# Kernel optimization log

Hardware: AMD Instinct MI355X
Metric: run time of the kernel (lower is better)

## Reference

```python
import jax, jax.numpy as jnp
import numpy as np

B, L, D = 4, 2048, 512
DK = D // 2
DH = 256.0  # scaling denominator


def _skew(QE):
    # QE: [B, L, M] with M == L (relative position logits via skewing trick)
    b, l, m = QE.shape
    pad = jnp.zeros((b, l, 1), QE.dtype)
    cat = jnp.concatenate([pad, QE], axis=2)      # [B, L, M+1]
    reshaped = cat.reshape(b, m + 1, l)           # [B, M+1, L]
    return reshaped[:, 1:, :]                     # [B, M, L]


def setup_inputs() -> dict:
    key = jax.random.key(0)
    ks = jax.random.split(key, 7)
    return {
        "inputQ": jax.random.normal(ks[0], (B, L, D), jnp.float32),
        "inputK": jax.random.normal(ks[1], (B, L, D), jnp.float32),
        "inputV": jax.random.normal(ks[2], (B, L, D), jnp.float32),
        "Wq": jax.random.normal(ks[3], (D, DK), jnp.float32) * 0.02,
        "Wk": jax.random.normal(ks[4], (D, DK), jnp.float32) * 0.02,
        "Wv": jax.random.normal(ks[5], (D, D), jnp.float32) * 0.02,
        "E": jax.random.normal(ks[6], (L, DK), jnp.float32) * 0.02,
    }


def reference(inputQ, inputK, inputV, Wq, Wk, Wv, E):
    Q = jnp.einsum('bld,dk->blk', inputQ, Wq)   # [B, L, DK]
    K = jnp.einsum('bld,dk->blk', inputK, Wk)   # [B, L, DK]
    V = jnp.einsum('bld,de->ble', inputV, Wv)   # [B, L, D]
    QE = jnp.einsum('blk,mk->blm', Q, E)        # [B, L, max_seq]
    Srel = _skew(QE)                             # [B, L, L]
    QKt = jnp.einsum('blk,bmk->blm', Q, K)      # [B, L, L]
    attn = jax.nn.softmax((QKt + Srel) / jnp.sqrt(jnp.float32(DH)), axis=-1)
    return jnp.einsum('blm,bme->ble', attn, V)  # [B, L, D]
```

## Files before the change

kernel.cpp:

```cpp
#include <hip/hip_runtime.h>
#include <hip/hip_bf16.h>

#define BB 4
#define LL 2048
#define DD 512
#define DKK 256

typedef __bf16 bf16;
typedef __bf16 bf16x4 __attribute__((ext_vector_type(4)));
typedef __bf16 bf16x8 __attribute__((ext_vector_type(8)));
typedef float f32x4 __attribute__((ext_vector_type(4)));

__device__ __forceinline__ void async_ld16(const bf16* g, bf16* l) {
    __builtin_amdgcn_global_load_lds(
        (const __attribute__((address_space(1))) void*)g,
        (__attribute__((address_space(3))) void*)l, 16, 0, 0);
}

__global__ void conv3_f32_bf16(const float* __restrict__ a, const float* __restrict__ bq,
                               const float* __restrict__ c,
                               bf16* __restrict__ oa, bf16* __restrict__ ob,
                               bf16* __restrict__ oc, int n4) {
    const float* in = (blockIdx.y == 0) ? a : (blockIdx.y == 1) ? bq : c;
    bf16* out = (blockIdx.y == 0) ? oa : (blockIdx.y == 1) ? ob : oc;
    int i = blockIdx.x * 256 + threadIdx.x;
    if (i < n4) {
        f32x4 v = *(const f32x4*)(in + (size_t)i * 4);
        bf16x4 o;
        #pragma unroll
        for (int j = 0; j < 4; ++j) o[j] = (bf16)v[j];
        *(bf16x4*)(out + (size_t)i * 4) = o;
    }
}

__global__ void prep_misc(const float* __restrict__ E, const float* __restrict__ Wq,
                          const float* __restrict__ Wk, const float* __restrict__ Wv,
                          bf16* __restrict__ Eb, bf16* __restrict__ WqT,
                          bf16* __restrict__ WkT, bf16* __restrict__ WvT) {
    int y = blockIdx.y;
    int idx = blockIdx.x * 256 + threadIdx.x;
    if (y == 0) {
        if (idx < (LL * DKK) / 4) {
            f32x4 v = *(const f32x4*)(E + (size_t)idx * 4);
            bf16x4 o;
            #pragma unroll
            for (int j = 0; j < 4; ++j) o[j] = (bf16)v[j];
            *(bf16x4*)(Eb + (size_t)idx * 4) = o;
        }
    } else if (y == 1) {
        if (idx < DD * DKK) { int r = idx / DKK, c = idx % DKK; WqT[(size_t)c * DD + r] = (bf16)Wq[idx]; }
    } else if (y == 2) {
        if (idx < DD * DKK) { int r = idx / DKK, c = idx % DKK; WkT[(size_t)c * DD + r] = (bf16)Wk[idx]; }
    } else {
        if (idx < DD * DD)  { int r = idx / DD,  c = idx % DD;  WvT[(size_t)c * DD + r] = (bf16)Wv[idx]; }
    }
}

template <int SKEW, int TRANSV>
__launch_bounds__(256, 2)
__global__ void gemm128(const bf16* __restrict__ A, const bf16* __restrict__ B,
                        bf16* __restrict__ C, int N, int K,
                        long aStride, long bStride, long cStride)
{
    __shared__ bf16 Als[128 * 32];
    __shared__ bf16 Bls[128 * 32];
    __shared__ bf16 tbuf[TRANSV ? 64 * 136 : 1];

    int tid  = threadIdx.x;
    int lane = tid & 63;
    int wid  = tid >> 6;
    int l15  = lane & 15;
    int quad = lane >> 4;
    int nb = N >> 7;
    int gx = blockIdx.x % nb;
    int gy = blockIdx.x / nb;

    const bf16* Ab = A + (size_t)blockIdx.y * aStride + (size_t)gy * 128 * K;
    const bf16* Bb = B + (size_t)blockIdx.y * bStride + (size_t)gx * 128 * K;

    int rl = lane >> 2;
    int sl = lane & 3;
    int half = wid & 1;
    const bf16* gsrc = (wid < 2) ? Ab : Bb;
    bf16* ldst = (wid < 2) ? Als : Bls;

    const bf16* gptr[4];
    #pragma unroll
    for (int u = 0; u < 4; ++u) {
        int inst = half * 4 + u;
        int row  = inst * 16 + rl;
        int c    = (sl - (row >> 1)) & 3;
        gptr[u] = gsrc + (size_t)row * K + c * 8;
    }

    f32x4 acc[4][4];
    #pragma unroll
    for (int i = 0; i < 4; ++i)
        #pragma unroll
        for (int j = 0; j < 4; ++j) acc[i][j] = 0;

    for (int k0 = 0; k0 < K; k0 += 32) {
        #pragma unroll
        for (int u = 0; u < 4; ++u) {
            async_ld16(gptr[u], ldst + (half * 4 + u) * 512);
            gptr[u] += 32;
        }
        __syncthreads();
        bf16x8 fA[4], fB[4];
        #pragma unroll
        for (int rt = 0; rt < 4; ++rt) {
            int row = (wid & 1) * 64 + rt * 16 + l15;
            int s   = (quad + (row >> 1)) & 3;
            fA[rt] = *(const bf16x8*)&Als[row * 32 + s * 8];
        }
        #pragma unroll
        for (int ct = 0; ct < 4; ++ct) {
            int col = (wid >> 1) * 64 + ct * 16 + l15;
            int s   = (quad + (col >> 1)) & 3;
            fB[ct] = *(const bf16x8*)&Bls[col * 32 + s * 8];
        }
        #pragma unroll
        for (int rt = 0; rt < 4; ++rt)
            #pragma unroll
            for (int ct = 0; ct < 4; ++ct)
                acc[rt][ct] = __builtin_amdgcn_mfma_f32_16x16x32_bf16(
                                  fA[rt], fB[ct], acc[rt][ct], 0, 0, 0);
        __syncthreads();
    }

    bf16* Cb = C + (size_t)blockIdx.y * cStride;
    int m0 = gy * 128 + (wid & 1) * 64;
    int n0 = gx * 128 + (wid >> 1) * 64;
    if (TRANSV) {
        #pragma unroll
        for (int p = 0; p < 2; ++p) {
            if ((wid >> 1) == p) {
                #pragma unroll
                for (int rt = 0; rt < 4; ++rt)
                    #pragma unroll
                    for (int ct = 0; ct < 4; ++ct)
                        #pragma unroll
                        for (int r = 0; r < 4; ++r)
                            tbuf[(ct * 16 + l15) * 136
                                 + (wid & 1) * 64 + rt * 16 + quad * 4 + r]
                                = (bf16)acc[rt][ct][r];
            }
            __syncthreads();
            int row = tid >> 2, c0 = (tid & 3) * 32;
            bf16* dst = C + (size_t)(gx * 128 + p * 64 + row) * (BB * LL)
                          + (size_t)gy * 128 + c0;
            #pragma unroll
            for (int q = 0; q < 4; ++q)
                *(bf16x8*)(dst + q * 8) = *(const bf16x8*)&tbuf[row * 136 + c0 + q * 8];
            __syncthreads();
        }
    } else if (!SKEW) {
        #pragma unroll
        for (int rt = 0; rt < 4; ++rt)
            #pragma unroll
            for (int ct = 0; ct < 4; ++ct)
                #pragma unroll
                for (int r = 0; r < 4; ++r) {
                    int m = m0 + rt * 16 + quad * 4 + r;
                    int n = n0 + ct * 16 + l15;
                    Cb[(size_t)m * N + n] = (bf16)acc[rt][ct][r];
                }
    } else {
        #pragma unroll
        for (int rt = 0; rt < 4; ++rt)
            #pragma unroll
            for (int ct = 0; ct < 4; ++ct)
                #pragma unroll
                for (int r = 0; r < 4; ++r) {
                    int row = m0 + rt * 16 + quad * 4 + r;
                    int c   = n0 + ct * 16 + l15;
                    bool lower = (c >= LL - 1 - row);
                    int dr = lower ? row : row - 1;
                    int dc = lower ? c - (LL - 1 - row) : c + row + 1;
                    if (lower || row >= 1)
                        Cb[(size_t)dr * LL + dc] = (bf16)acc[rt][ct][r];
                }
    }
}

__launch_bounds__(256, 2)
__global__ void attn_kernel(const bf16* __restrict__ Qw, const bf16* __restrict__ Kw,
                            const bf16* __restrict__ Vt, const bf16* __restrict__ Srel,
                            float* __restrict__ out)
{
    __shared__ bf16  Klds[64 * 256];
    __shared__ bf16  Vlds[256 * 64];
    __shared__ bf16  SrelL[2][32 * 72];
    __shared__ bf16  Ps[32][72];
    __shared__ float pmax[32][4];
    __shared__ float aSt[32];

    int tid  = threadIdx.x;
    int lane = tid & 63;
    int wid  = tid >> 6;
    int l15  = lane & 15;
    int quad = lane >> 4;

    int xcd = blockIdx.x & 7;
    int b   = xcd >> 1;
    int dh  = xcd & 1;
    int i0  = (blockIdx.x >> 3) * 32;

    const bf16* Qb = Qw + (size_t)b * LL * DKK;
    const bf16* Kb = Kw + (size_t)b * LL * DKK;
    const bf16* Sb = Srel + (size_t)b * LL * LL;
    const bf16* Vb = Vt + (size_t)(dh * 256) * (BB * LL) + (size_t)b * LL;

    const bf16* kptr[8];
    const bf16* vptr[8];
    #pragma unroll
    for (int u = 0; u < 8; ++u) {
        int inst = wid * 8 + u;
        int j_ = inst * 2 + (lane >> 5);
        int ck = ((lane & 31) - j_) & 31;
        kptr[u] = Kb + (size_t)j_ * DKK + ck * 8;
        int d_ = inst * 8 + (lane >> 3);
        int cv = ((lane & 7) - d_) & 7;
        vptr[u] = Vb + (size_t)d_ * (BB * LL) + cv * 8;
    }

    bf16x8 Qreg[2][8];
    #pragma unroll
    for (int rt = 0; rt < 2; ++rt)
        #pragma unroll
        for (int ks = 0; ks < 8; ++ks)
            Qreg[rt][ks] = *(const bf16x8*)(Qb + (size_t)(i0 + rt * 16 + l15) * DKK
                                            + ks * 32 + quad * 8);

    f32x4 accO[2][4];
    #pragma unroll
    for (int rt = 0; rt < 2; ++rt)
        #pragma unroll
        for (int nt = 0; nt < 4; ++nt) accO[rt][nt] = 0;

    float mreg0 = -1e30f, mreg1 = -1e30f;
    float lreg0 = 0.f, lreg1 = 0.f;

    int srow = i0 + (tid >> 3), ssg = tid & 7;
    bf16x8 srelNext = *(const bf16x8*)(Sb + (size_t)srow * LL + ssg * 8);
    const bf16* sPtr = Sb + (size_t)srow * LL + ssg * 8 + 64;
    __builtin_amdgcn_sched_barrier(0);
    #pragma unroll
    for (int u = 0; u < 8; ++u) {
        async_ld16(kptr[u], Klds + (wid * 8 + u) * 512);
        kptr[u] += 64 * DKK;
    }
    __builtin_amdgcn_sched_barrier(0);
    #pragma unroll
    for (int u = 0; u < 8; ++u) {
        async_ld16(vptr[u], Vlds + (wid * 8 + u) * 512);
        vptr[u] += 64;
    }
    __builtin_amdgcn_sched_barrier(0);
    *(bf16x8*)&SrelL[0][(tid >> 3) * 72 + (tid & 7) * 8] = srelNext;
    asm volatile("s_waitcnt lgkmcnt(0)\ns_barrier" ::: "memory");

    int jrow = wid * 16 + l15;

    for (int j0 = 0; j0 < LL; j0 += 64) {
        bool notlast = (j0 + 64 < LL);
        int p = (j0 >> 6) & 1;

        asm volatile("s_waitcnt vmcnt(8)" ::: "memory");
        bf16x8 kf[8];
        #pragma unroll
        for (int ks = 0; ks < 8; ++ks) {
            int cp = (ks * 4 + quad + jrow) & 31;
            kf[ks] = *(const bf16x8*)&Klds[jrow * 256 + cp * 8];
        }
        asm volatile("s_waitcnt lgkmcnt(0)" ::: "memory");
        __builtin_amdgcn_sched_barrier(0);
        if (notlast) {
            srelNext = *(const bf16x8*)sPtr;
            sPtr += 64;
        }
        __builtin_amdgcn_sched_barrier(0);
        if (notlast) {
            #pragma unroll
            for (int u = 0; u < 8; ++u) {
                async_ld16(kptr[u], Klds + (wid * 8 + u) * 512);
                kptr[u] += 64 * DKK;
            }
        }
        __builtin_amdgcn_sched_barrier(0);

        f32x4 s0 = 0, s1 = 0;
        __builtin_amdgcn_s_setprio(1);
        #pragma unroll
        for (int ks = 0; ks < 8; ++ks) {
            s0 = __builtin_amdgcn_mfma_f32_16x16x32_bf16(kf[ks], Qreg[0][ks], s0, 0, 0, 0);
            s1 = __builtin_amdgcn_mfma_f32_16x16x32_bf16(kf[ks], Qreg[1][ks], s1, 0, 0, 0);
        }
        __builtin_amdgcn_s_setprio(0);

        bf16x4 sr0 = *(const bf16x4*)&SrelL[p][l15 * 72 + wid * 16 + quad * 4];
        bf16x4 sr1 = *(const bf16x4*)&SrelL[p][(16 + l15) * 72 + wid * 16 + quad * 4];
        int jb = j0 + wid * 16 + quad * 4;
        float v0[4], v1[4];
        #pragma unroll
        for (int r = 0; r < 4; ++r) {
            float a0 = (jb + r == i0 + l15 + 1)      ? 0.f : (float)sr0[r];
            float a1 = (jb + r == i0 + 16 + l15 + 1) ? 0.f : (float)sr1[r];
            v0[r] = (s0[r] + a0) * 0.0625f;
            v1[r] = (s1[r] + a1) * 0.0625f;
        }
        float m0 = fmaxf(fmaxf(v0[0], v0[1]), fmaxf(v0[2], v0[3]));
        float m1 = fmaxf(fmaxf(v1[0], v1[1]), fmaxf(v1[2], v1[3]));
        m0 = fmaxf(m0, __shfl_xor(m0, 16)); m0 = fmaxf(m0, __shfl_xor(m0, 32));
        m1 = fmaxf(m1, __shfl_xor(m1, 16)); m1 = fmaxf(m1, __shfl_xor(m1, 32));
        if (quad == 0) { pmax[l15][wid] = m0; pmax[16 + l15][wid] = m1; }
        asm volatile("s_waitcnt lgkmcnt(0)\ns_barrier" ::: "memory");

        f32x4 pm0 = *(const f32x4*)&pmax[l15][0];
        f32x4 pm1 = *(const f32x4*)&pmax[16 + l15][0];
        float mf0 = fmaxf(fmaxf(fmaxf(pm0[0], pm0[1]), fmaxf(pm0[2], pm0[3])), mreg0);
        float mf1 = fmaxf(fmaxf(fmaxf(pm1[0], pm1[1]), fmaxf(pm1[2], pm1[3])), mreg1);
        float al0 = __expf(mreg0 - mf0); mreg0 = mf0;
        float al1 = __expf(mreg1 - mf1); mreg1 = mf1;
        if (notlast)
            *(bf16x8*)&SrelL[p ^ 1][(tid >> 3) * 72 + (tid & 7) * 8] = srelNext;
        float ps0 = 0.f, ps1 = 0.f;
        bf16x4 pv0, pv1;
        #pragma unroll
        for (int r = 0; r < 4; ++r) {
            float e0 = __expf(v0[r] - mf0); ps0 += e0; pv0[r] = (bf16)e0;
            float e1 = __expf(v1[r] - mf1); ps1 += e1; pv1[r] = (bf16)e1;
        }
        ps0 += __shfl_xor(ps0, 16); ps0 += __shfl_xor(ps0, 32);
        ps1 += __shfl_xor(ps1, 16); ps1 += __shfl_xor(ps1, 32);
        lreg0 = al0 * lreg0 + ps0;
        lreg1 = al1 * lreg1 + ps1;
        *(bf16x4*)&Ps[l15][wid * 16 + quad * 4]      = pv0;
        *(bf16x4*)&Ps[16 + l15][wid * 16 + quad * 4] = pv1;
        if (wid == 0 && quad == 0) { aSt[l15] = al0; aSt[16 + l15] = al1; }
        asm volatile("s_waitcnt lgkmcnt(0)\ns_barrier" ::: "memory");

        if (notlast) asm volatile("s_waitcnt vmcnt(8)" ::: "memory");
        else         asm volatile("s_waitcnt vmcnt(0)" ::: "memory");
        bf16x8 aF[2][2];
        #pragma unroll
        for (int rt = 0; rt < 2; ++rt)
            #pragma unroll
            for (int kk = 0; kk < 2; ++kk)
                aF[rt][kk] = *(const bf16x8*)&Ps[rt * 16 + l15][kk * 32 + quad * 8];
        float ar[2][4];
        #pragma unroll
        for (int rt = 0; rt < 2; ++rt)
            #pragma unroll
            for (int r = 0; r < 4; ++r) ar[rt][r] = aSt[rt * 16 + quad * 4 + r];
        bf16x8 vf[4][2];
        #pragma unroll
        for (int nt = 0; nt < 4; ++nt) {
            int dd = wid * 64 + nt * 16 + l15;
            int c0 = (quad + dd) & 7;
            int c1 = (4 + quad + dd) & 7;
            vf[nt][0] = *(const bf16x8*)&Vlds[dd * 64 + c0 * 8];
            vf[nt][1] = *(const bf16x8*)&Vlds[dd * 64 + c1 * 8];
        }
        asm volatile("s_waitcnt lgkmcnt(0)" ::: "memory");
        __builtin_amdgcn_sched_barrier(0);
        if (notlast) {
            #pragma unroll
            for (int u = 0; u < 8; ++u) {
                async_ld16(vptr[u], Vlds + (wid * 8 + u) * 512);
                vptr[u] += 64;
            }
        }
        __builtin_amdgcn_sched_barrier(0);
        __builtin_amdgcn_s_setprio(1);
        #pragma unroll
        for (int nt = 0; nt < 4; ++nt) {
            #pragma unroll
            for (int rt = 0; rt < 2; ++rt) {
                f32x4 o = accO[rt][nt];
                o[0] *= ar[rt][0]; o[1] *= ar[rt][1];
                o[2] *= ar[rt][2]; o[3] *= ar[rt][3];
                o = __builtin_amdgcn_mfma_f32_16x16x32_bf16(aF[rt][0], vf[nt][0], o, 0, 0, 0);
                o = __builtin_amdgcn_mfma_f32_16x16x32_bf16(aF[rt][1], vf[nt][1], o, 0, 0, 0);
                accO[rt][nt] = o;
            }
        }
        __builtin_amdgcn_s_setprio(0);
    }

    if (quad == 0) { pmax[l15][wid] = lreg0; pmax[16 + l15][wid] = lreg1; }
    asm volatile("s_waitcnt lgkmcnt(0)\ns_barrier" ::: "memory");
    float lr[2][4];
    #pragma unroll
    for (int rt = 0; rt < 2; ++rt)
        #pragma unroll
        for (int r = 0; r < 4; ++r) {
            f32x4 lp = *(const f32x4*)&pmax[rt * 16 + quad * 4 + r][0];
            lr[rt][r] = 1.f / (lp[0] + lp[1] + lp[2] + lp[3]);
        }
    #pragma unroll
    for (int rt = 0; rt < 2; ++rt)
        #pragma unroll
        for (int nt = 0; nt < 4; ++nt)
            #pragma unroll
            for (int r = 0; r < 4; ++r) {
                int i = i0 + rt * 16 + quad * 4 + r;
                int d = dh * 256 + wid * 64 + nt * 16 + l15;
                out[((size_t)b * LL + i) * DD + d] = accO[rt][nt][r] * lr[rt][r];
            }
}

extern "C" void kernel_launch(void* const* d_in, const int* in_sizes, int n_in,
                              void* d_out, int out_size, void* d_ws, size_t ws_size,
                              hipStream_t stream) {
    const float* inQ = (const float*)d_in[0];
    const float* inK = (const float*)d_in[1];
    const float* inV = (const float*)d_in[2];
    const float* Wq  = (const float*)d_in[3];
    const float* Wk  = (const float*)d_in[4];
    const float* Wv  = (const float*)d_in[5];
    const float* E   = (const float*)d_in[6];
    float* out = (float*)d_out;

    char* ws = (char*)d_ws;
    bf16* Qw   = (bf16*)(ws);
    bf16* Kw   = (bf16*)(ws + ((size_t)4  << 20));
    bf16* Vt   = (bf16*)(ws + ((size_t)8  << 20));
    bf16* SrelW= (bf16*)(ws + ((size_t)16 << 20));
    bf16* Xq   = (bf16*)(ws + ((size_t)16 << 20));
    bf16* Xk   = (bf16*)(ws + ((size_t)24 << 20));
    bf16* Xv   = (bf16*)(ws + ((size_t)32 << 20));
    bf16* WqT  = (bf16*)(ws + ((size_t)48 << 20));
    bf16* WkT  = (bf16*)(ws + ((size_t)48 << 20) + 262144);
    bf16* WvT  = (bf16*)(ws + ((size_t)48 << 20) + 524288);
    bf16* Eb   = (bf16*)(ws + ((size_t)49 << 20));

    conv3_f32_bf16<<<dim3(4096, 3), 256, 0, stream>>>(inQ, inK, inV, Xq, Xk, Xv,
                                                      (BB * LL * DD) / 4);
    prep_misc<<<dim3(1024, 4), 256, 0, stream>>>(E, Wq, Wk, Wv, Eb, WqT, WkT, WvT);

    gemm128<0, 0><<<dim3(2 * 64, 2),  256, 0, stream>>>(Xq, WqT, Qw, DKK, DD,
                                                        4194304L, 131072L, 2097152L);
    gemm128<0, 1><<<dim3(4 * 64, 1),  256, 0, stream>>>(Xv, WvT, Vt, DD, DD, 0, 0, 0);
    gemm128<1, 0><<<dim3(16 * 16, BB), 256, 0, stream>>>(Qw, Eb, SrelW, LL, DKK,
                                                         (long)LL * DKK, 0, (long)LL * LL);
    attn_kernel<<<dim3(BB * 64 * 2), 256, 0, stream>>>(Qw, Kw, Vt, SrelW, out);
}
```

Measured before the change: 234.7 us.

## Merge Q/K/V projection GEMMs into one launch and software-pipeline PV in attention

The Q, K and V projection GEMMs now run in a single kernel that picks its mode from the block index, replacing two launches with one 512-block launch. The Srel GEMM moves into its own specialized kernel. In the attention loop, the P·V product for the previous tile now runs after the next QK^T step, which lets the Srel buffer shrink to a single LDS slot. The aim is to cut launch overhead and overlap the V loads with QK^T compute, at the cost of more complex vmcnt accounting and an extra epilogue MFMA pass.

```diff
diff --git a/kernel.cpp b/kernel.cpp
--- a/kernel.cpp
+++ b/kernel.cpp
@@ -56,27 +56,37 @@
     }
 }
 
-template <int SKEW, int TRANSV>
 __launch_bounds__(256, 2)
-__global__ void gemm128(const bf16* __restrict__ A, const bf16* __restrict__ B,
-                        bf16* __restrict__ C, int N, int K,
-                        long aStride, long bStride, long cStride)
+__global__ void gemm_qkv(const bf16* __restrict__ Xq, const bf16* __restrict__ WqT,
+                         bf16* __restrict__ Qw,
+                         const bf16* __restrict__ Xk, const bf16* __restrict__ WkT,
+                         bf16* __restrict__ Kw,
+                         const bf16* __restrict__ Xv, const bf16* __restrict__ WvT,
+                         bf16* __restrict__ Vt)
 {
     __shared__ bf16 Als[128 * 32];
     __shared__ bf16 Bls[128 * 32];
-    __shared__ bf16 tbuf[TRANSV ? 64 * 136 : 1];
+    __shared__ bf16 tbuf[64 * 136];
 
     int tid  = threadIdx.x;
     int lane = tid & 63;
     int wid  = tid >> 6;
     int l15  = lane & 15;
     int quad = lane >> 4;
-    int nb = N >> 7;
-    int gx = blockIdx.x % nb;
-    int gy = blockIdx.x / nb;
-
-    const bf16* Ab = A + (size_t)blockIdx.y * aStride + (size_t)gy * 128 * K;
-    const bf16* Bb = B + (size_t)blockIdx.y * bStride + (size_t)gx * 128 * K;
+
+    int bid  = blockIdx.x;
+    int mode = (bid < 128) ? 0 : (bid < 256) ? 1 : 2;
+    int idx  = bid - ((mode == 0) ? 0 : (mode == 1) ? 128 : 256);
+    int nb   = (mode == 2) ? 4 : 2;
+    int gx = idx % nb;
+    int gy = idx / nb;
+    int N  = (mode == 2) ? DD : DKK;
+    const bf16* A  = (mode == 0) ? Xq  : (mode == 1) ? Xk  : Xv;
+    const bf16* Bw = (mode == 0) ? WqT : (mode == 1) ? WkT : WvT;
+    const int K = DD;
+
+    const bf16* Ab = A + (size_t)gy * 128 * K;
+    const bf16* Bb = Bw + (size_t)gx * 128 * K;
 
     int rl = lane >> 2;
     int sl = lane & 3;
@@ -128,10 +138,7 @@
         __syncthreads();
     }
 
-    bf16* Cb = C + (size_t)blockIdx.y * cStride;
-    int m0 = gy * 128 + (wid & 1) * 64;
-    int n0 = gx * 128 + (wid >> 1) * 64;
-    if (TRANSV) {
+    if (mode == 2) {
         #pragma unroll
         for (int p = 0; p < 2; ++p) {
             if ((wid >> 1) == p) {
@@ -147,14 +154,17 @@
             }
             __syncthreads();
             int row = tid >> 2, c0 = (tid & 3) * 32;
-            bf16* dst = C + (size_t)(gx * 128 + p * 64 + row) * (BB * LL)
-                          + (size_t)gy * 128 + c0;
+            bf16* dst = Vt + (size_t)(gx * 128 + p * 64 + row) * (BB * LL)
+                           + (size_t)gy * 128 + c0;
             #pragma unroll
             for (int q = 0; q < 4; ++q)
                 *(bf16x8*)(dst + q * 8) = *(const bf16x8*)&tbuf[row * 136 + c0 + q * 8];
             __syncthreads();
         }
-    } else if (!SKEW) {
+    } else {
+        bf16* Cb = (mode == 0) ? Qw : Kw;
+        int m0 = gy * 128 + (wid & 1) * 64;
+        int n0 = gx * 128 + (wid >> 1) * 64;
         #pragma unroll
         for (int rt = 0; rt < 4; ++rt)
             #pragma unroll
@@ -165,22 +175,96 @@
                     int n = n0 + ct * 16 + l15;
                     Cb[(size_t)m * N + n] = (bf16)acc[rt][ct][r];
                 }
-    } else {
+    }
+}
+
+__launch_bounds__(256, 2)
+__global__ void gemm_srel(const bf16* __restrict__ A, const bf16* __restrict__ B,
+                          bf16* __restrict__ C, long aStride, long cStride)
+{
+    __shared__ bf16 Als[128 * 32];
+    __shared__ bf16 Bls[128 * 32];
+
+    int tid  = threadIdx.x;
+    int lane = tid & 63;
+    int wid  = tid >> 6;
+    int l15  = lane & 15;
+    int quad = lane >> 4;
+    const int N = LL, K = DKK;
+    int nb = N >> 7;
+    int gx = blockIdx.x % nb;
+    int gy = blockIdx.x / nb;
+
+    const bf16* Ab = A + (size_t)blockIdx.y * aStride + (size_t)gy * 128 * K;
+    const bf16* Bb = B + (size_t)gx * 128 * K;
+
+    int rl = lane >> 2;
+    int sl = lane & 3;
+    int half = wid & 1;
+    const bf16* gsrc = (wid < 2) ? Ab : Bb;
+    bf16* ldst = (wid < 2) ? Als : Bls;
+
+    const bf16* gptr[4];
+    #pragma unroll
+    for (int u = 0; u < 4; ++u) {
+        int inst = half * 4 + u;
+        int row  = inst * 16 + rl;
+        int c    = (sl - (row >> 1)) & 3;
+        gptr[u] = gsrc + (size_t)row * K + c * 8;
+    }
+
+    f32x4 acc[4][4];
+    #pragma unroll
+    for (int i = 0; i < 4; ++i)
+        #pragma unroll
+        for (int j = 0; j < 4; ++j) acc[i][j] = 0;
+
+    for (int k0 = 0; k0 < K; k0 += 32) {
+        #pragma unroll
+        for (int u = 0; u < 4; ++u) {
+            async_ld16(gptr[u], ldst + (half * 4 + u) * 512);
+            gptr[u] += 32;
+        }
+        __syncthreads();
+        bf16x8 fA[4], fB[4];
+        #pragma unroll
+        for (int rt = 0; rt < 4; ++rt) {
+            int row = (wid & 1) * 64 + rt * 16 + l15;
+            int s   = (quad + (row >> 1)) & 3;
+            fA[rt] = *(const bf16x8*)&Als[row * 32 + s * 8];
+        }
+        #pragma unroll
+        for (int ct = 0; ct < 4; ++ct) {
+            int col = (wid >> 1) * 64 + ct * 16 + l15;
+            int s   = (quad + (col >> 1)) & 3;
+            fB[ct] = *(const bf16x8*)&Bls[col * 32 + s * 8];
+        }
         #pragma unroll
         for (int rt = 0; rt < 4; ++rt)
             #pragma unroll
             for (int ct = 0; ct < 4; ++ct)
-                #pragma unroll
-                for (int r = 0; r < 4; ++r) {
-                    int row = m0 + rt * 16 + quad * 4 + r;
-                    int c   = n0 + ct * 16 + l15;
-                    bool lower = (c >= LL - 1 - row);
-                    int dr = lower ? row : row - 1;
-                    int dc = lower ? c - (LL - 1 - row) : c + row + 1;
-                    if (lower || row >= 1)
-                        Cb[(size_t)dr * LL + dc] = (bf16)acc[rt][ct][r];
-                }
-    }
+                acc[rt][ct] = __builtin_amdgcn_mfma_f32_16x16x32_bf16(
+                                  fA[rt], fB[ct], acc[rt][ct], 0, 0, 0);
+        __syncthreads();
+    }
+
+    bf16* Cb = C + (size_t)blockIdx.y * cStride;
+    int m0 = gy * 128 + (wid & 1) * 64;
+    int n0 = gx * 128 + (wid >> 1) * 64;
+    #pragma unroll
+    for (int rt = 0; rt < 4; ++rt)
+        #pragma unroll
+        for (int ct = 0; ct < 4; ++ct)
+            #pragma unroll
+            for (int r = 0; r < 4; ++r) {
+                int row = m0 + rt * 16 + quad * 4 + r;
+                int c   = n0 + ct * 16 + l15;
+                bool lower = (c >= LL - 1 - row);
+                int dr = lower ? row : row - 1;
+                int dc = lower ? c - (LL - 1 - row) : c + row + 1;
+                if (lower || row >= 1)
+                    Cb[(size_t)dr * LL + dc] = (bf16)acc[rt][ct][r];
+            }
 }
 
 __launch_bounds__(256, 2)
@@ -190,7 +274,7 @@
 {
     __shared__ bf16  Klds[64 * 256];
     __shared__ bf16  Vlds[256 * 64];
-    __shared__ bf16  SrelL[2][32 * 72];
+    __shared__ bf16  SrelL[32 * 72];
     __shared__ bf16  Ps[32][72];
     __shared__ float pmax[32][4];
     __shared__ float aSt[32];
@@ -241,6 +325,8 @@
     float mreg0 = -1e30f, mreg1 = -1e30f;
     float lreg0 = 0.f, lreg1 = 0.f;
 
+    asm volatile("s_waitcnt vmcnt(0)" ::: "memory");
+
     int srow = i0 + (tid >> 3), ssg = tid & 7;
     bf16x8 srelNext = *(const bf16x8*)(Sb + (size_t)srow * LL + ssg * 8);
     const bf16* sPtr = Sb + (size_t)srow * LL + ssg * 8 + 64;
@@ -251,22 +337,16 @@
         kptr[u] += 64 * DKK;
     }
     __builtin_amdgcn_sched_barrier(0);
-    #pragma unroll
-    for (int u = 0; u < 8; ++u) {
-        async_ld16(vptr[u], Vlds + (wid * 8 + u) * 512);
-        vptr[u] += 64;
-    }
-    __builtin_amdgcn_sched_barrier(0);
-    *(bf16x8*)&SrelL[0][(tid >> 3) * 72 + (tid & 7) * 8] = srelNext;
+    *(bf16x8*)&SrelL[(tid >> 3) * 72 + (tid & 7) * 8] = srelNext;
     asm volatile("s_waitcnt lgkmcnt(0)\ns_barrier" ::: "memory");
 
     int jrow = wid * 16 + l15;
 
     for (int j0 = 0; j0 < LL; j0 += 64) {
         bool notlast = (j0 + 64 < LL);
-        int p = (j0 >> 6) & 1;
-
-        asm volatile("s_waitcnt vmcnt(8)" ::: "memory");
+
+        if (j0 == 0) asm volatile("s_waitcnt vmcnt(0)" ::: "memory");
+        else         asm volatile("s_waitcnt vmcnt(8)" ::: "memory");
         bf16x8 kf[8];
         #pragma unroll
         for (int ks = 0; ks < 8; ++ks) {
@@ -298,8 +378,61 @@
         }
         __builtin_amdgcn_s_setprio(0);
 
-        bf16x4 sr0 = *(const bf16x4*)&SrelL[p][l15 * 72 + wid * 16 + quad * 4];
-        bf16x4 sr1 = *(const bf16x4*)&SrelL[p][(16 + l15) * 72 + wid * 16 + quad * 4];
+        if (notlast) asm volatile("s_waitcnt vmcnt(9)" ::: "memory");
+        else         asm volatile("s_waitcnt vmcnt(0)" ::: "memory");
+        if (j0) {
+            bf16x8 aF[2][2];
+            #pragma unroll
+            for (int rt = 0; rt < 2; ++rt)
+                #pragma unroll
+                for (int kk = 0; kk < 2; ++kk)
+                    aF[rt][kk] = *(const bf16x8*)&Ps[rt * 16 + l15][kk * 32 + quad * 8];
+            float ar[2][4];
+            #pragma unroll
+            for (int rt = 0; rt < 2; ++rt)
+                #pragma unroll
+                for (int r = 0; r < 4; ++r) ar[rt][r] = aSt[rt * 16 + quad * 4 + r];
+            bf16x8 vf[4][2];
+            #pragma unroll
+            for (int nt = 0; nt < 4; ++nt) {
+                int dd = wid * 64 + nt * 16 + l15;
+                int c0 = (quad + dd) & 7;
+                int c1 = (4 + quad + dd) & 7;
+                vf[nt][0] = *(const bf16x8*)&Vlds[dd * 64 + c0 * 8];
+                vf[nt][1] = *(const bf16x8*)&Vlds[dd * 64 + c1 * 8];
+            }
+            asm volatile("s_waitcnt lgkmcnt(0)" ::: "memory");
+            __builtin_amdgcn_sched_barrier(0);
+            #pragma unroll
+            for (int u = 0; u < 8; ++u) {
+                async_ld16(vptr[u], Vlds + (wid * 8 + u) * 512);
+                vptr[u] += 64;
+            }
+            __builtin_amdgcn_sched_barrier(0);
+            __builtin_amdgcn_s_setprio(1);
+            #pragma unroll
+            for (int nt = 0; nt < 4; ++nt) {
+                #pragma unroll
+                for (int rt = 0; rt < 2; ++rt) {
+                    f32x4 o = accO[rt][nt];
+                    o[0] *= ar[rt][0]; o[1] *= ar[rt][1];
+                    o[2] *= ar[rt][2]; o[3] *= ar[rt][3];
+                    o = __builtin_amdgcn_mfma_f32_16x16x32_bf16(aF[rt][0], vf[nt][0], o, 0, 0, 0);
+                    o = __builtin_amdgcn_mfma_f32_16x16x32_bf16(aF[rt][1], vf[nt][1], o, 0, 0, 0);
+                    accO[rt][nt] = o;
+                }
+            }
+            __builtin_amdgcn_s_setprio(0);
+        } else {
+            #pragma unroll
+            for (int u = 0; u < 8; ++u) {
+                async_ld16(vptr[u], Vlds + (wid * 8 + u) * 512);
+                vptr[u] += 64;
+            }
+        }
+
+        bf16x4 sr0 = *(const bf16x4*)&SrelL[l15 * 72 + wid * 16 + quad * 4];
+        bf16x4 sr1 = *(const bf16x4*)&SrelL[(16 + l15) * 72 + wid * 16 + quad * 4];
         int jb = j0 + wid * 16 + quad * 4;
         float v0[4], v1[4];
         #pragma unroll
@@ -323,7 +456,7 @@
         float al0 = __expf(mreg0 - mf0); mreg0 = mf0;
         float al1 = __expf(mreg1 - mf1); mreg1 = mf1;
         if (notlast)
-            *(bf16x8*)&SrelL[p ^ 1][(tid >> 3) * 72 + (tid & 7) * 8] = srelNext;
+            *(bf16x8*)&SrelL[(tid >> 3) * 72 + (tid & 7) * 8] = srelNext;
         float ps0 = 0.f, ps1 = 0.f;
         bf16x4 pv0, pv1;
         #pragma unroll
@@ -339,9 +472,10 @@
         *(bf16x4*)&Ps[16 + l15][wid * 16 + quad * 4] = pv1;
         if (wid == 0 && quad == 0) { aSt[l15] = al0; aSt[16 + l15] = al1; }
         asm volatile("s_waitcnt lgkmcnt(0)\ns_barrier" ::: "memory");
-
-        if (notlast) asm volatile("s_waitcnt vmcnt(8)" ::: "memory");
-        else         asm volatile("s_waitcnt vmcnt(0)" ::: "memory");
+    }
+
+    asm volatile("s_waitcnt vmcnt(0)" ::: "memory");
+    {
         bf16x8 aF[2][2];
         #pragma unroll
         for (int rt = 0; rt < 2; ++rt)
@@ -362,17 +496,6 @@
             vf[nt][0] = *(const bf16x8*)&Vlds[dd * 64 + c0 * 8];
             vf[nt][1] = *(const bf16x8*)&Vlds[dd * 64 + c1 * 8];
         }
-        asm volatile("s_waitcnt lgkmcnt(0)" ::: "memory");
-        __builtin_amdgcn_sched_barrier(0);
-        if (notlast) {
-            #pragma unroll
-            for (int u = 0; u < 8; ++u) {
-                async_ld16(vptr[u], Vlds + (wid * 8 + u) * 512);
-                vptr[u] += 64;
-            }
-        }
-        __builtin_amdgcn_sched_barrier(0);
-        __builtin_amdgcn_s_setprio(1);
         #pragma unroll
         for (int nt = 0; nt < 4; ++nt) {
             #pragma unroll
@@ -385,7 +508,6 @@
                 accO[rt][nt] = o;
             }
         }
-        __builtin_amdgcn_s_setprio(0);
     }
 
     if (quad == 0) { pmax[l15][wid] = lreg0; pmax[16 + l15][wid] = lreg1; }
@@ -439,10 +561,8 @@
                                                       (BB * LL * DD) / 4);
     prep_misc<<<dim3(1024, 4), 256, 0, stream>>>(E, Wq, Wk, Wv, Eb, WqT, WkT, WvT);
 
-    gemm128<0, 0><<<dim3(2 * 64, 2),  256, 0, stream>>>(Xq, WqT, Qw, DKK, DD,
-                                                        4194304L, 131072L, 2097152L);
-    gemm128<0, 1><<<dim3(4 * 64, 1),  256, 0, stream>>>(Xv, WvT, Vt, DD, DD, 0, 0, 0);
-    gemm128<1, 0><<<dim3(16 * 16, BB), 256, 0, stream>>>(Qw, Eb, SrelW, LL, DKK,
-                                                         (long)LL * DKK, 0, (long)LL * LL);
+    gemm_qkv<<<512, 256, 0, stream>>>(Xq, WqT, Qw, Xk, WkT, Kw, Xv, WvT, Vt);
+    gemm_srel<<<dim3(16 * 16, BB), 256, 0, stream>>>(Qw, Eb, SrelW,
+                                                     (long)LL * DKK, (long)LL * LL);
     attn_kernel<<<dim3(BB * 64 * 2), 256, 0, stream>>>(Qw, Kw, Vt, SrelW, out);
 }
```

Measured after the change: 229.7 us. 1.02x faster.
